# Kernel optimization log

Measured on AMD Instinct MI355X. Metric: run time of the kernel, lower is better.

Reference implementation:

```python
import jax, jax.numpy as jnp
import numpy as np

SIGMA_DEG = 2.5
EPS = 1e-8


def setup_inputs() -> dict:
    key = jax.random.key(0)
    k1, k2 = jax.random.split(key)
    b, t, o = 4, 16, 32
    # trajectory points: lat in [-90, 90], lon in [-180, 180]
    lat_pts = jax.random.uniform(k1, (b, t, o, 1), jnp.float32, -90.0, 90.0)
    lon_pts = jax.random.uniform(k2, (b, t, o, 1), jnp.float32, -180.0, 180.0)
    traj = jnp.concatenate([lat_pts, lon_pts], axis=-1)  # (b, t, o, 2)
    lat = jnp.linspace(-90.0, 90.0, 181, dtype=jnp.float32)   # (h,)
    lon = jnp.linspace(-180.0, 180.0, 360, dtype=jnp.float32)  # (w,)
    return {"traj": traj, "lat": lat, "lon": lon}


def reference(traj, lat, lon):
    # traj: (b,t,o,2), lat: (h,), lon: (w,)
    inv_sigma2 = 1.0 / (SIGMA_DEG ** 2 + EPS)
    lat_t = traj[..., 0][:, :, :, None, None]  # (b,t,o,1,1)
    lon_t = traj[..., 1][:, :, :, None, None]
    d2 = ((lat[None, None, None, :, None] - lat_t) ** 2
          + (lon[None, None, None, None, :] - lon_t) ** 2) * inv_sigma2  # (b,t,o,h,w)
    heat = jnp.exp(-0.5 * d2).sum(axis=2)  # (b,t,h,w)
    heat = heat / (jnp.max(heat, axis=(-2, -1), keepdims=True) + EPS)
    return heat
```

## Files before the change

kernel.cpp:

```cpp
#include <hip/hip_runtime.h>
#include <hip/hip_bf16.h>


#define NH 181
#define NW 360
#define NO 32
#define NIMG 64
#define NCHUNK 4
#define ROWS_PER_CHUNK 46

__global__ __launch_bounds__(384) void traj_raster_kernel(
    const float* __restrict__ traj,
    const float* __restrict__ lat,
    const float* __restrict__ lon,
    float* __restrict__ out,
    unsigned int* __restrict__ maxbuf
) {
    const int img = blockIdx.x;
    const int chunk = blockIdx.y;
    const int tid = threadIdx.x;

    __shared__ float fs[NO][NH];
    __shared__ float gs[NO][NW];
    __shared__ float wavemax[6];

    const float inv_sigma2 = 1.0f / (2.5f * 2.5f + 1e-8f);

    for (int i = tid; i < NO * NH; i += 384) {
        const int o = i / NH, h = i - o * NH;
        const float d = lat[h] - traj[(img * NO + o) * 2 + 0];
        fs[o][h] = __expf(-0.5f * inv_sigma2 * d * d);
    }
    for (int i = tid; i < NO * NW; i += 384) {
        const int o = i / NW, w = i - o * NW;
        const float d = lon[w] - traj[(img * NO + o) * 2 + 1];
        gs[o][w] = __expf(-0.5f * inv_sigma2 * d * d);
    }
    __syncthreads();

    float lmax = 0.0f;
    const int w = tid;
    if (w < NW) {
        float greg[NO];
        #pragma unroll
        for (int o = 0; o < NO; ++o) greg[o] = gs[o][w];

        const int h0 = chunk * ROWS_PER_CHUNK;
        const int h1 = min(h0 + ROWS_PER_CHUNK, NH);
        float* __restrict__ outp = out + (size_t)img * NH * NW;

        for (int h = h0; h < h1; ++h) {
            float acc = 0.0f;
            #pragma unroll
            for (int o = 0; o < NO; ++o) {
                acc += greg[o] * fs[o][h];
            }
            outp[h * NW + w] = acc;
            lmax = fmaxf(lmax, acc);
        }
    }

    #pragma unroll
    for (int off = 32; off > 0; off >>= 1) {
        lmax = fmaxf(lmax, __shfl_down(lmax, off, 64));
    }
    if ((tid & 63) == 0) wavemax[tid >> 6] = lmax;
    __syncthreads();
    if (tid == 0) {
        float m = wavemax[0];
        #pragma unroll
        for (int i = 1; i < 6; ++i) m = fmaxf(m, wavemax[i]);
        atomicMax(&maxbuf[img], __float_as_uint(m));
    }
}

__global__ __launch_bounds__(256) void traj_norm_kernel(
    float* __restrict__ out,
    const unsigned int* __restrict__ maxbuf
) {
    const int PIX4_PER_IMG = NH * NW / 4;
    const int TOT4 = NIMG * PIX4_PER_IMG;
    int i4 = blockIdx.x * blockDim.x + threadIdx.x;
    if (i4 >= TOT4) return;
    const int img = i4 / PIX4_PER_IMG;
    const float m = __uint_as_float(maxbuf[img]);
    const float s = 1.0f / (m + 1e-8f);
    float4 v = ((float4*)out)[i4];
    v.x *= s; v.y *= s; v.z *= s; v.w *= s;
    ((float4*)out)[i4] = v;
}

extern "C" void kernel_launch(void* const* d_in, const int* in_sizes, int n_in,
                              void* d_out, int out_size, void* d_ws, size_t ws_size,
                              hipStream_t stream) {
    const float* traj = (const float*)d_in[0];
    const float* lat  = (const float*)d_in[1];
    const float* lon  = (const float*)d_in[2];
    float* out = (float*)d_out;
    unsigned int* maxbuf = (unsigned int*)d_ws;

    hipMemsetAsync(maxbuf, 0, NIMG * sizeof(unsigned int), stream);

    dim3 gridA(NIMG, NCHUNK);
    traj_raster_kernel<<<gridA, 384, 0, stream>>>(traj, lat, lon, out, maxbuf);

    const int TOT4 = NIMG * NH * NW / 4;
    traj_norm_kernel<<<(TOT4 + 255) / 256, 256, 0, stream>>>(out, maxbuf);
}
```

Measured before the change: 89.62 us.

## Recompute heatmap in two passes instead of writing then renormalizing output

Replaces the write-then-rescale scheme with two launches of a templated kernel. The first pass computes the separable Gaussian sum only to find per-chunk maxima, with no output writes. The second pass folds the normalization scale into the longitude factors and writes final values once. It also register-tiles the outer product (8 rows by 8 columns per thread, float4 LDS loads and stores) and drops the memset and atomics. This trades an extra compute pass for eliminating the full read-modify-write of the output.

```diff
diff --git a/kernel.cpp b/kernel.cpp
--- a/kernel.cpp
+++ b/kernel.cpp
@@ -1,93 +1,120 @@
 #include <hip/hip_runtime.h>
-#include <hip/hip_bf16.h>
 
 
 #define NH 181
 #define NW 360
 #define NO 32
 #define NIMG 64
-#define NCHUNK 4
-#define ROWS_PER_CHUNK 46
+#define NCH 6
+#define CROWS 32
+#define TM 8
+#define NTX 45
+#define TY 4
+#define NTHR 192
 
-__global__ __launch_bounds__(384) void traj_raster_kernel(
+__device__ __forceinline__ float img_scale(const float* __restrict__ maxbuf, int img) {
+    float m = 0.0f;
+    #pragma unroll
+    for (int c = 0; c < NCH; ++c) m = fmaxf(m, maxbuf[img * NCH + c]);
+    return 1.0f / (m + 1e-8f);
+}
+
+template <bool WRITE>
+__global__ __launch_bounds__(NTHR) void traj_pass(
     const float* __restrict__ traj,
     const float* __restrict__ lat,
     const float* __restrict__ lon,
     float* __restrict__ out,
-    unsigned int* __restrict__ maxbuf
+    float* __restrict__ maxbuf
 ) {
     const int img = blockIdx.x;
     const int chunk = blockIdx.y;
     const int tid = threadIdx.x;
 
-    __shared__ float fs[NO][NH];
+    __shared__ float fs[NO][CROWS];
     __shared__ float gs[NO][NW];
-    __shared__ float wavemax[6];
+    __shared__ float red[NTHR / 64];
 
-    const float inv_sigma2 = 1.0f / (2.5f * 2.5f + 1e-8f);
+    const float C = -0.5f / (2.5f * 2.5f + 1e-8f);
+    const float scale = WRITE ? img_scale(maxbuf, img) : 1.0f;
 
-    for (int i = tid; i < NO * NH; i += 384) {
-        const int o = i / NH, h = i - o * NH;
-        const float d = lat[h] - traj[(img * NO + o) * 2 + 0];
-        fs[o][h] = __expf(-0.5f * inv_sigma2 * d * d);
+    for (int i = tid; i < NO * CROWS; i += NTHR) {
+        const int k = i >> 5, r = i & 31;
+        const int row = chunk * CROWS + r;
+        float v = 0.0f;
+        if (row < NH) {
+            const float d = lat[row] - traj[(img * NO + k) * 2 + 0];
+            v = __expf(C * d * d);
+        }
+        fs[k][r] = v;
     }
-    for (int i = tid; i < NO * NW; i += 384) {
-        const int o = i / NW, w = i - o * NW;
-        const float d = lon[w] - traj[(img * NO + o) * 2 + 1];
-        gs[o][w] = __expf(-0.5f * inv_sigma2 * d * d);
+    for (int i = tid; i < NO * NW; i += NTHR) {
+        const int k = i / NW, w = i - k * NW;
+        const float d = lon[w] - traj[(img * NO + k) * 2 + 1];
+        gs[k][w] = __expf(C * d * d) * scale;
     }
     __syncthreads();
 
     float lmax = 0.0f;
-    const int w = tid;
-    if (w < NW) {
-        float greg[NO];
+    if (tid < NTX * TY) {
+        const int tx = tid % NTX, ty = tid / NTX;
+        const int w0 = tx * 4;
+        const int r0 = ty * TM;
+
+        float acc[TM][8];
         #pragma unroll
-        for (int o = 0; o < NO; ++o) greg[o] = gs[o][w];
+        for (int i = 0; i < TM; ++i)
+            #pragma unroll
+            for (int j = 0; j < 8; ++j) acc[i][j] = 0.0f;
 
-        const int h0 = chunk * ROWS_PER_CHUNK;
-        const int h1 = min(h0 + ROWS_PER_CHUNK, NH);
-        float* __restrict__ outp = out + (size_t)img * NH * NW;
+        #pragma unroll 2
+        for (int k = 0; k < NO; ++k) {
+            const float4 gA = *(const float4*)&gs[k][w0];
+            const float4 gB = *(const float4*)&gs[k][w0 + 180];
+            const float4 fA = *(const float4*)&fs[k][r0];
+            const float4 fB = *(const float4*)&fs[k][r0 + 4];
+            const float fr[TM] = {fA.x, fA.y, fA.z, fA.w, fB.x, fB.y, fB.z, fB.w};
+            const float gr[8]  = {gA.x, gA.y, gA.z, gA.w, gB.x, gB.y, gB.z, gB.w};
+            #pragma unroll
+            for (int i = 0; i < TM; ++i)
+                #pragma unroll
+                for (int j = 0; j < 8; ++j)
+                    acc[i][j] += fr[i] * gr[j];
+        }
 
-        for (int h = h0; h < h1; ++h) {
-            float acc = 0.0f;
+        if (WRITE) {
+            float* __restrict__ op = out + (size_t)img * NH * NW;
             #pragma unroll
-            for (int o = 0; o < NO; ++o) {
-                acc += greg[o] * fs[o][h];
+            for (int i = 0; i < TM; ++i) {
+                const int r = chunk * CROWS + r0 + i;
+                if (r < NH) {
+                    const float4 vA = {acc[i][0], acc[i][1], acc[i][2], acc[i][3]};
+                    const float4 vB = {acc[i][4], acc[i][5], acc[i][6], acc[i][7]};
+                    *(float4*)&op[r * NW + w0] = vA;
+                    *(float4*)&op[r * NW + w0 + 180] = vB;
+                }
             }
-            outp[h * NW + w] = acc;
-            lmax = fmaxf(lmax, acc);
+        } else {
+            #pragma unroll
+            for (int i = 0; i < TM; ++i) {
+                const int r = chunk * CROWS + r0 + i;
+                if (r < NH) {
+                    #pragma unroll
+                    for (int j = 0; j < 8; ++j) lmax = fmaxf(lmax, acc[i][j]);
+                }
+            }
         }
     }
 
-    #pragma unroll
-    for (int off = 32; off > 0; off >>= 1) {
-        lmax = fmaxf(lmax, __shfl_down(lmax, off, 64));
+    if (!WRITE) {
+        #pragma unroll
+        for (int off = 32; off > 0; off >>= 1)
+            lmax = fmaxf(lmax, __shfl_down(lmax, off, 64));
+        if ((tid & 63) == 0) red[tid >> 6] = lmax;
+        __syncthreads();
+        if (tid == 0)
+            maxbuf[img * NCH + chunk] = fmaxf(fmaxf(red[0], red[1]), red[2]);
     }
-    if ((tid & 63) == 0) wavemax[tid >> 6] = lmax;
-    __syncthreads();
-    if (tid == 0) {
-        float m = wavemax[0];
-        #pragma unroll
-        for (int i = 1; i < 6; ++i) m = fmaxf(m, wavemax[i]);
-        atomicMax(&maxbuf[img], __float_as_uint(m));
-    }
-}
-
-__global__ __launch_bounds__(256) void traj_norm_kernel(
-    float* __restrict__ out,
-    const unsigned int* __restrict__ maxbuf
-) {
-    const int PIX4_PER_IMG = NH * NW / 4;
-    const int TOT4 = NIMG * PIX4_PER_IMG;
-    int i4 = blockIdx.x * blockDim.x + threadIdx.x;
-    if (i4 >= TOT4) return;
-    const int img = i4 / PIX4_PER_IMG;
-    const float m = __uint_as_float(maxbuf[img]);
-    const float s = 1.0f / (m + 1e-8f);
-    float4 v = ((float4*)out)[i4];
-    v.x *= s; v.y *= s; v.z *= s; v.w *= s;
-    ((float4*)out)[i4] = v;
 }
 
 extern "C" void kernel_launch(void* const* d_in, const int* in_sizes, int n_in,
@@ -97,13 +124,9 @@
     const float* lat  = (const float*)d_in[1];
     const float* lon  = (const float*)d_in[2];
     float* out = (float*)d_out;
-    unsigned int* maxbuf = (unsigned int*)d_ws;
+    float* maxbuf = (float*)d_ws;
 
-    hipMemsetAsync(maxbuf, 0, NIMG * sizeof(unsigned int), stream);
-
-    dim3 gridA(NIMG, NCHUNK);
-    traj_raster_kernel<<<gridA, 384, 0, stream>>>(traj, lat, lon, out, maxbuf);
-
-    const int TOT4 = NIMG * NH * NW / 4;
-    traj_norm_kernel<<<(TOT4 + 255) / 256, 256, 0, stream>>>(out, maxbuf);
+    dim3 grid(NIMG, NCH);
+    traj_pass<false><<<grid, NTHR, 0, stream>>>(traj, lat, lon, out, maxbuf);
+    traj_pass<true><<<grid, NTHR, 0, stream>>>(traj, lat, lon, out, maxbuf);
 }
```

After: 90.01 us. No clear change (+0.4%).
